# Performance work log

Measured on AMD Instinct MI355X. Metric: run time of the kernel, lower is better.

Reference implementation:

```python
import jax, jax.numpy as jnp
import numpy as np

BETA = 0.25


def setup_inputs() -> dict:
    key = jax.random.key(0)
    k1, k2 = jax.random.split(key)
    x = jax.random.normal(k1, (32, 64, 64, 64), dtype=jnp.float32)
    # tf.random_uniform_initializer default: uniform in [-0.05, 0.05]
    embeddings = jax.random.uniform(k2, (64, 512), dtype=jnp.float32, minval=-0.05, maxval=0.05)
    return {"x": x, "embeddings": embeddings}


def reference(x, embeddings):
    D = embeddings.shape[0]
    flat = x.reshape(-1, D)  # [N, D]
    # squared euclidean distances via the matmul expansion: [N, K]
    distances = (
        jnp.sum(flat * flat, axis=1, keepdims=True)
        - 2.0 * (flat @ embeddings)
        + jnp.sum(embeddings * embeddings, axis=0, keepdims=True)
    )
    codes = jnp.argmin(distances, axis=1)  # [N]
    # direct gather of codebook rows (math-equivalent to one_hot @ embeddings.T)
    quantized = embeddings.T[codes].reshape(x.shape)
    loss = (
        jnp.mean((jax.lax.stop_gradient(x) - quantized) ** 2)
        + BETA * jnp.mean((x - jax.lax.stop_gradient(quantized)) ** 2)
    )
    # straight-through estimator
    out = x + jax.lax.stop_gradient(quantized - x)
    return out, loss
```

## Files before the change

kernel.cpp:

```cpp
#include <hip/hip_runtime.h>
#include <cstddef>

#define D 64
#define K 512
#define NROWS (32*64*64)
#define RPB 64
#define NBLK (NROWS / RPB)
#define NOUT 8388608


__global__ __launch_bounds__(256) void vq_prep(const float* __restrict__ emb,
                                               float* __restrict__ eT,
                                               float* __restrict__ enorm) {
    const int k = blockIdx.x * blockDim.x + threadIdx.x;
    if (k >= K) return;
    float nrm = 0.f;
#pragma unroll
    for (int d = 0; d < D; ++d) {
        const float v = emb[d * K + k];
        nrm = __fadd_rn(nrm, __fmul_rn(v, v));
        eT[k * D + d] = v;
    }
    enorm[k] = nrm;
}

__global__ __launch_bounds__(256) void vq_main(const float* __restrict__ x,
                                               const float* __restrict__ eT,
                                               const float* __restrict__ enorm,
                                               float* __restrict__ out,
                                               float* __restrict__ partials) {
    __shared__ float xT[D][RPB];
    __shared__ float s_dist[256];
    __shared__ int   s_idx[256];
    __shared__ int   s_code[RPB];
    __shared__ float s_red[4];

    const int t    = threadIdx.x;
    const int wave = t >> 6;
    const int lane = t & 63;
    const size_t rowbase = (size_t)blockIdx.x * RPB;

    {
        const float4* __restrict__ src = (const float4*)(x + (rowbase + lane) * D + wave * 16);
        const float4 v0 = src[0], v1 = src[1], v2 = src[2], v3 = src[3];
        const int d0 = wave * 16;
        xT[d0+ 0][lane] = v0.x; xT[d0+ 1][lane] = v0.y; xT[d0+ 2][lane] = v0.z; xT[d0+ 3][lane] = v0.w;
        xT[d0+ 4][lane] = v1.x; xT[d0+ 5][lane] = v1.y; xT[d0+ 6][lane] = v1.z; xT[d0+ 7][lane] = v1.w;
        xT[d0+ 8][lane] = v2.x; xT[d0+ 9][lane] = v2.y; xT[d0+10][lane] = v2.z; xT[d0+11][lane] = v2.w;
        xT[d0+12][lane] = v3.x; xT[d0+13][lane] = v3.y; xT[d0+14][lane] = v3.z; xT[d0+15][lane] = v3.w;
    }
    __syncthreads();

    float r0, r1, r2, r3, r4, r5, r6, r7;
    {
        float v;
        v = xT[0][lane]; r0 = __fmul_rn(v, v);
        v = xT[1][lane]; r1 = __fmul_rn(v, v);
        v = xT[2][lane]; r2 = __fmul_rn(v, v);
        v = xT[3][lane]; r3 = __fmul_rn(v, v);
        v = xT[4][lane]; r4 = __fmul_rn(v, v);
        v = xT[5][lane]; r5 = __fmul_rn(v, v);
        v = xT[6][lane]; r6 = __fmul_rn(v, v);
        v = xT[7][lane]; r7 = __fmul_rn(v, v);
#pragma unroll
        for (int b = 1; b < 8; ++b) {
            v = xT[8*b+0][lane]; r0 = __fadd_rn(r0, __fmul_rn(v, v));
            v = xT[8*b+1][lane]; r1 = __fadd_rn(r1, __fmul_rn(v, v));
            v = xT[8*b+2][lane]; r2 = __fadd_rn(r2, __fmul_rn(v, v));
            v = xT[8*b+3][lane]; r3 = __fadd_rn(r3, __fmul_rn(v, v));
            v = xT[8*b+4][lane]; r4 = __fadd_rn(r4, __fmul_rn(v, v));
            v = xT[8*b+5][lane]; r5 = __fadd_rn(r5, __fmul_rn(v, v));
            v = xT[8*b+6][lane]; r6 = __fadd_rn(r6, __fmul_rn(v, v));
            v = xT[8*b+7][lane]; r7 = __fadd_rn(r7, __fmul_rn(v, v));
        }
    }
    const float xnorm = __fadd_rn(__fadd_rn(__fadd_rn(r0, r1), __fadd_rn(r2, r3)),
                                  __fadd_rn(__fadd_rn(r4, r5), __fadd_rn(r6, r7)));

    const int kbase = __builtin_amdgcn_readfirstlane(wave << 7);
    float best = 3.4028235e38f;
    int   bidx = 0;
#pragma unroll 1
    for (int g = 0; g < 16; ++g) {
        const int kc = kbase + g * 8;
        const float* __restrict__ eg = eT + (size_t)kc * D;
        float acc[8][4];
#pragma unroll
        for (int c = 0; c < 8; ++c) {
            acc[c][0] = 0.f; acc[c][1] = 0.f; acc[c][2] = 0.f; acc[c][3] = 0.f;
        }
#pragma unroll
        for (int j = 0; j < 16; ++j) {
            const float x0 = xT[4*j+0][lane];
            const float x1 = xT[4*j+1][lane];
            const float x2 = xT[4*j+2][lane];
            const float x3 = xT[4*j+3][lane];
#pragma unroll
            for (int c = 0; c < 8; ++c) {
                const float4 v = *(const float4*)(eg + (size_t)c * D + 4*j);
                acc[c][0] = fmaf(x0, v.x, acc[c][0]);
                acc[c][1] = fmaf(x1, v.y, acc[c][1]);
                acc[c][2] = fmaf(x2, v.z, acc[c][2]);
                acc[c][3] = fmaf(x3, v.w, acc[c][3]);
            }
        }
#pragma unroll
        for (int c = 0; c < 8; ++c) {
            const float dot = __fadd_rn(__fadd_rn(acc[c][0], acc[c][1]),
                                        __fadd_rn(acc[c][2], acc[c][3]));
            const float dd = __fadd_rn(__fsub_rn(xnorm, __fmul_rn(2.f, dot)), enorm[kc + c]);
            if (dd < best) { best = dd; bidx = kc + c; }
        }
    }

    s_dist[t] = best;
    s_idx[t]  = bidx;
    __syncthreads();
    if (t < RPB) {
        float bb = s_dist[t];
        int   bi = s_idx[t];
#pragma unroll
        for (int w = 1; w < 4; ++w) {
            const float ob = s_dist[w * 64 + t];
            const int   oi = s_idx[w * 64 + t];
            if (ob < bb) { bb = ob; bi = oi; }
        }
        s_code[t] = bi;
    }
    __syncthreads();

    const int c   = t & 15;
    const int r0i = t >> 4;
    float lacc = 0.f;
#pragma unroll
    for (int i = 0; i < 4; ++i) {
        const int r = r0i + 16 * i;
        const int code = s_code[r];
        const float4 q = *(const float4*)(eT + (size_t)code * D + 4 * c);
        const float4 b = *(const float4*)(x + (rowbase + r) * D + 4 * c);
        const float f0 = __fsub_rn(b.x, q.x), f1 = __fsub_rn(b.y, q.y);
        const float f2 = __fsub_rn(b.z, q.z), f3 = __fsub_rn(b.w, q.w);
        lacc = fmaf(f0, f0, lacc); lacc = fmaf(f1, f1, lacc);
        lacc = fmaf(f2, f2, lacc); lacc = fmaf(f3, f3, lacc);
        float4 o;
        o.x = __fadd_rn(b.x, __fsub_rn(q.x, b.x));
        o.y = __fadd_rn(b.y, __fsub_rn(q.y, b.y));
        o.z = __fadd_rn(b.z, __fsub_rn(q.z, b.z));
        o.w = __fadd_rn(b.w, __fsub_rn(q.w, b.w));
        *(float4*)(out + (rowbase + r) * D + 4 * c) = o;
    }

#pragma unroll
    for (int off = 32; off > 0; off >>= 1) lacc += __shfl_down(lacc, off);
    if (lane == 0) s_red[wave] = lacc;
    __syncthreads();
    if (t == 0) partials[blockIdx.x] = (s_red[0] + s_red[1]) + (s_red[2] + s_red[3]);
}

__global__ __launch_bounds__(256) void vq_finish(const float* __restrict__ partials,
                                                 float* __restrict__ loss_out) {
    __shared__ float s_red[4];
    const int t = threadIdx.x;
    float a = 0.f;
#pragma unroll
    for (int i = 0; i < 8; ++i) a += partials[t + 256 * i];
#pragma unroll
    for (int off = 32; off > 0; off >>= 1) a += __shfl_down(a, off);
    if ((t & 63) == 0) s_red[t >> 6] = a;
    __syncthreads();
    if (t == 0) {
        const float S = (s_red[0] + s_red[1]) + (s_red[2] + s_red[3]);
        const float m = S / (float)NOUT;
        loss_out[0] = m + 0.25f * m;
    }
}

extern "C" void kernel_launch(void* const* d_in, const int* in_sizes, int n_in,
                              void* d_out, int out_size, void* d_ws, size_t ws_size,
                              hipStream_t stream) {
    const float* x   = (const float*)d_in[0];
    const float* emb = (const float*)d_in[1];
    float* out = (float*)d_out;
    float* ws  = (float*)d_ws;

    float* eT       = ws;
    float* enorm    = ws + 32768;
    float* partials = ws + 32768 + 512;

    vq_prep<<<2, 256, 0, stream>>>(emb, eT, enorm);
    vq_main<<<NBLK, 256, 0, stream>>>(x, eT, enorm, out, partials);
    vq_finish<<<1, 256, 0, stream>>>(partials, out + NOUT);
}
```

Measured before the change: 236.4 us.

## Store x tile row-major with padding and fuse loss reduction via atomics

Changes the shared-memory x tile from a transposed [D][RPB] layout to row-major with a padded stride of 68. Each thread can then read its row with float4 loads instead of scalar loads, which cuts LDS instruction count in the distance loop. The inner j loop is only partially unrolled, which lowers register pressure but adds loop overhead. The separate finish kernel is replaced by per-block atomicAdd into a global sum plus a last-block-done counter, saving one launch at the cost of 2048 contended atomics and a nondeterministic float summation order.

```diff
diff --git a/kernel.cpp b/kernel.cpp
--- a/kernel.cpp
+++ b/kernel.cpp
@@ -7,12 +7,16 @@
 #define RPB 64
 #define NBLK (NROWS / RPB)
 #define NOUT 8388608
+#define XSTR 68
 
 
 __global__ __launch_bounds__(256) void vq_prep(const float* __restrict__ emb,
                                                float* __restrict__ eT,
-                                               float* __restrict__ enorm) {
+                                               float* __restrict__ enorm,
+                                               float* __restrict__ lsum,
+                                               unsigned* __restrict__ done) {
     const int k = blockIdx.x * blockDim.x + threadIdx.x;
+    if (k == 0) { *lsum = 0.f; *done = 0u; }
     if (k >= K) return;
     float nrm = 0.f;
 #pragma unroll
@@ -28,8 +32,9 @@
                                                const float* __restrict__ eT,
                                                const float* __restrict__ enorm,
                                                float* __restrict__ out,
-                                               float* __restrict__ partials) {
-    __shared__ float xT[D][RPB];
+                                               float* __restrict__ lsum,
+                                               unsigned* __restrict__ done) {
+    __shared__ float xT[RPB * XSTR];
     __shared__ float s_dist[256];
     __shared__ int   s_idx[256];
     __shared__ int   s_code[RPB];
@@ -43,35 +48,36 @@
     {
         const float4* __restrict__ src = (const float4*)(x + (rowbase + lane) * D + wave * 16);
         const float4 v0 = src[0], v1 = src[1], v2 = src[2], v3 = src[3];
-        const int d0 = wave * 16;
-        xT[d0+ 0][lane] = v0.x; xT[d0+ 1][lane] = v0.y; xT[d0+ 2][lane] = v0.z; xT[d0+ 3][lane] = v0.w;
-        xT[d0+ 4][lane] = v1.x; xT[d0+ 5][lane] = v1.y; xT[d0+ 6][lane] = v1.z; xT[d0+ 7][lane] = v1.w;
-        xT[d0+ 8][lane] = v2.x; xT[d0+ 9][lane] = v2.y; xT[d0+10][lane] = v2.z; xT[d0+11][lane] = v2.w;
-        xT[d0+12][lane] = v3.x; xT[d0+13][lane] = v3.y; xT[d0+14][lane] = v3.z; xT[d0+15][lane] = v3.w;
+        float* dst = &xT[lane * XSTR + wave * 16];
+        *(float4*)(dst +  0) = v0;
+        *(float4*)(dst +  4) = v1;
+        *(float4*)(dst +  8) = v2;
+        *(float4*)(dst + 12) = v3;
     }
     __syncthreads();
 
+    const float* __restrict__ xrow = &xT[lane * XSTR];
+
     float r0, r1, r2, r3, r4, r5, r6, r7;
     {
-        float v;
-        v = xT[0][lane]; r0 = __fmul_rn(v, v);
-        v = xT[1][lane]; r1 = __fmul_rn(v, v);
-        v = xT[2][lane]; r2 = __fmul_rn(v, v);
-        v = xT[3][lane]; r3 = __fmul_rn(v, v);
-        v = xT[4][lane]; r4 = __fmul_rn(v, v);
-        v = xT[5][lane]; r5 = __fmul_rn(v, v);
-        v = xT[6][lane]; r6 = __fmul_rn(v, v);
-        v = xT[7][lane]; r7 = __fmul_rn(v, v);
+        const float4 ca = *(const float4*)(xrow + 0);
+        const float4 cb = *(const float4*)(xrow + 4);
+        r0 = __fmul_rn(ca.x, ca.x); r1 = __fmul_rn(ca.y, ca.y);
+        r2 = __fmul_rn(ca.z, ca.z); r3 = __fmul_rn(ca.w, ca.w);
+        r4 = __fmul_rn(cb.x, cb.x); r5 = __fmul_rn(cb.y, cb.y);
+        r6 = __fmul_rn(cb.z, cb.z); r7 = __fmul_rn(cb.w, cb.w);
 #pragma unroll
         for (int b = 1; b < 8; ++b) {
-            v = xT[8*b+0][lane]; r0 = __fadd_rn(r0, __fmul_rn(v, v));
-            v = xT[8*b+1][lane]; r1 = __fadd_rn(r1, __fmul_rn(v, v));
-            v = xT[8*b+2][lane]; r2 = __fadd_rn(r2, __fmul_rn(v, v));
-            v = xT[8*b+3][lane]; r3 = __fadd_rn(r3, __fmul_rn(v, v));
-            v = xT[8*b+4][lane]; r4 = __fadd_rn(r4, __fmul_rn(v, v));
-            v = xT[8*b+5][lane]; r5 = __fadd_rn(r5, __fmul_rn(v, v));
-            v = xT[8*b+6][lane]; r6 = __fadd_rn(r6, __fmul_rn(v, v));
-            v = xT[8*b+7][lane]; r7 = __fadd_rn(r7, __fmul_rn(v, v));
+            const float4 da = *(const float4*)(xrow + 8*b);
+            const float4 db = *(const float4*)(xrow + 8*b + 4);
+            r0 = __fadd_rn(r0, __fmul_rn(da.x, da.x));
+            r1 = __fadd_rn(r1, __fmul_rn(da.y, da.y));
+            r2 = __fadd_rn(r2, __fmul_rn(da.z, da.z));
+            r3 = __fadd_rn(r3, __fmul_rn(da.w, da.w));
+            r4 = __fadd_rn(r4, __fmul_rn(db.x, db.x));
+            r5 = __fadd_rn(r5, __fmul_rn(db.y, db.y));
+            r6 = __fadd_rn(r6, __fmul_rn(db.z, db.z));
+            r7 = __fadd_rn(r7, __fmul_rn(db.w, db.w));
         }
     }
     const float xnorm = __fadd_rn(__fadd_rn(__fadd_rn(r0, r1), __fadd_rn(r2, r3)),
@@ -84,30 +90,27 @@
     for (int g = 0; g < 16; ++g) {
         const int kc = kbase + g * 8;
         const float* __restrict__ eg = eT + (size_t)kc * D;
-        float acc[8][4];
+        float a[8][4];
 #pragma unroll
         for (int c = 0; c < 8; ++c) {
-            acc[c][0] = 0.f; acc[c][1] = 0.f; acc[c][2] = 0.f; acc[c][3] = 0.f;
+            a[c][0] = 0.f; a[c][1] = 0.f; a[c][2] = 0.f; a[c][3] = 0.f;
         }
-#pragma unroll
+#pragma unroll 2
         for (int j = 0; j < 16; ++j) {
-            const float x0 = xT[4*j+0][lane];
-            const float x1 = xT[4*j+1][lane];
-            const float x2 = xT[4*j+2][lane];
-            const float x3 = xT[4*j+3][lane];
+            const float4 xv = *(const float4*)(xrow + 4 * j);
 #pragma unroll
             for (int c = 0; c < 8; ++c) {
-                const float4 v = *(const float4*)(eg + (size_t)c * D + 4*j);
-                acc[c][0] = fmaf(x0, v.x, acc[c][0]);
-                acc[c][1] = fmaf(x1, v.y, acc[c][1]);
-                acc[c][2] = fmaf(x2, v.z, acc[c][2]);
-                acc[c][3] = fmaf(x3, v.w, acc[c][3]);
+                const float4 ev = *(const float4*)(eg + c * D + 4 * j);
+                a[c][0] = fmaf(xv.x, ev.x, a[c][0]);
+                a[c][1] = fmaf(xv.y, ev.y, a[c][1]);
+                a[c][2] = fmaf(xv.z, ev.z, a[c][2]);
+                a[c][3] = fmaf(xv.w, ev.w, a[c][3]);
             }
         }
 #pragma unroll
         for (int c = 0; c < 8; ++c) {
-            const float dot = __fadd_rn(__fadd_rn(acc[c][0], acc[c][1]),
-                                        __fadd_rn(acc[c][2], acc[c][3]));
+            const float dot = __fadd_rn(__fadd_rn(a[c][0], a[c][1]),
+                                        __fadd_rn(a[c][2], a[c][3]));
             const float dd = __fadd_rn(__fsub_rn(xnorm, __fmul_rn(2.f, dot)), enorm[kc + c]);
             if (dd < best) { best = dd; bidx = kc + c; }
         }
@@ -129,15 +132,15 @@
     }
     __syncthreads();
 
-    const int c   = t & 15;
+    const int ch  = t & 15;
     const int r0i = t >> 4;
     float lacc = 0.f;
 #pragma unroll
     for (int i = 0; i < 4; ++i) {
         const int r = r0i + 16 * i;
         const int code = s_code[r];
-        const float4 q = *(const float4*)(eT + (size_t)code * D + 4 * c);
-        const float4 b = *(const float4*)(x + (rowbase + r) * D + 4 * c);
+        const float4 q = *(const float4*)(eT + (size_t)code * D + 4 * ch);
+        const float4 b = *(const float4*)(x + (rowbase + r) * D + 4 * ch);
         const float f0 = __fsub_rn(b.x, q.x), f1 = __fsub_rn(b.y, q.y);
         const float f2 = __fsub_rn(b.z, q.z), f3 = __fsub_rn(b.w, q.w);
         lacc = fmaf(f0, f0, lacc); lacc = fmaf(f1, f1, lacc);
@@ -147,31 +150,23 @@
         o.y = __fadd_rn(b.y, __fsub_rn(q.y, b.y));
         o.z = __fadd_rn(b.z, __fsub_rn(q.z, b.z));
         o.w = __fadd_rn(b.w, __fsub_rn(q.w, b.w));
-        *(float4*)(out + (rowbase + r) * D + 4 * c) = o;
+        *(float4*)(out + (rowbase + r) * D + 4 * ch) = o;
     }
 
 #pragma unroll
     for (int off = 32; off > 0; off >>= 1) lacc += __shfl_down(lacc, off);
     if (lane == 0) s_red[wave] = lacc;
     __syncthreads();
-    if (t == 0) partials[blockIdx.x] = (s_red[0] + s_red[1]) + (s_red[2] + s_red[3]);
-}
-
-__global__ __launch_bounds__(256) void vq_finish(const float* __restrict__ partials,
-                                                 float* __restrict__ loss_out) {
-    __shared__ float s_red[4];
-    const int t = threadIdx.x;
-    float a = 0.f;
-#pragma unroll
-    for (int i = 0; i < 8; ++i) a += partials[t + 256 * i];
-#pragma unroll
-    for (int off = 32; off > 0; off >>= 1) a += __shfl_down(a, off);
-    if ((t & 63) == 0) s_red[t >> 6] = a;
-    __syncthreads();
     if (t == 0) {
-        const float S = (s_red[0] + s_red[1]) + (s_red[2] + s_red[3]);
-        const float m = S / (float)NOUT;
-        loss_out[0] = m + 0.25f * m;
+        const float part = (s_red[0] + s_red[1]) + (s_red[2] + s_red[3]);
+        atomicAdd(lsum, part);
+        __threadfence();
+        const unsigned prev = atomicAdd(done, 1u);
+        if (prev == NBLK - 1) {
+            const float total = atomicAdd(lsum, 0.f);
+            const float mm = total / (float)NOUT;
+            out[NOUT] = mm + 0.25f * mm;
+        }
     }
 }
 
@@ -183,11 +178,11 @@
     float* out = (float*)d_out;
     float* ws  = (float*)d_ws;
 
-    float* eT       = ws;
-    float* enorm    = ws + 32768;
-    float* partials = ws + 32768 + 512;
+    float*    eT    = ws;
+    float*    enorm = ws + 32768;
+    float*    lsum  = ws + 33280;
+    unsigned* done  = (unsigned*)(ws + 33281);
 
-    vq_prep<<<2, 256, 0, stream>>>(emb, eT, enorm);
-    vq_main<<<NBLK, 256, 0, stream>>>(x, eT, enorm, out, partials);
-    vq_finish<<<1, 256, 0, stream>>>(partials, out + NOUT);
+    vq_prep<<<2, 256, 0, stream>>>(emb, eT, enorm, lsum, done);
+    vq_main<<<NBLK, 256, 0, stream>>>(x, eT, enorm, out, lsum, done);
 }
```

Result: slower. 294.6 us (+24.6%).
